# Kernel optimization log

Measured on AMD Instinct MI355X. Metric: run time of the kernel, lower is better.

The kernel has to match this reference:

```python
import jax, jax.numpy as jnp
import numpy as np

T = 200000


def _sine_layer(tvec, A, w, phi, phic, wc):
    # tvec: (t,), A/w/phi: (n,1), phic/wc: (1,)
    phi_static = jax.nn.relu(phic)  # (1,)
    w_static = jax.nn.relu(wc)
    ph = jax.nn.relu(phi) + phi_static  # (n,1)
    ww = jax.nn.relu(w) + w_static
    sine = A * jnp.sin(ww * tvec[None, :] + ph)  # (n,t)
    return sine, phi_static, w_static


def _selector_layer(tvec, wave_input, w, phi, phic, wc, phi_prev, w_prev):
    # wave_input: (n,t), w/phi: (m,n), phic/wc/phi_prev/w_prev: (1,)
    # NOTE: phi_prev/w_prev passed but phi_prev flag is False in the network,
    # so they are NOT added (matches torch: `if self.phi_prev and ...`).
    phi_static = jax.nn.relu(phic)
    w_static = jax.nn.relu(wc)
    ph = (jax.nn.relu(phi) + phi_static)[:, :, None]  # (m,n,1)
    ww = (jax.nn.relu(w) + w_static)[:, :, None]
    sine = 0.5 * jnp.sin(ww * tvec[None, None, :] + ph) + 0.5  # (m,n,t)
    out = jnp.einsum('mnt,nt->mt', sine, wave_input)  # (m,t)
    return out, phi_static, w_static


def setup_inputs() -> dict:
    key = jax.random.key(0)
    ks = jax.random.split(key, 18)
    r = lambda k, s: jax.random.normal(k, s, dtype=jnp.float32)
    return {
        'initial_wave_input': r(ks[0], (20, T)),
        'A0': r(ks[1], (20, 1)), 'w0': r(ks[2], (20, 1)), 'phi0': r(ks[3], (20, 1)),
        'wc0': r(ks[4], (1,)), 'phic0': r(ks[5], (1,)),
        'w1': r(ks[6], (25, 20)), 'phi1': r(ks[7], (25, 20)),
        'wc1': r(ks[8], (1,)), 'phic1': r(ks[9], (1,)),
        'w2': r(ks[10], (30, 25)), 'phi2': r(ks[11], (30, 25)),
        'wc2': r(ks[12], (1,)), 'phic2': r(ks[13], (1,)),
        'w3': r(ks[14], (1, 30)), 'phi3': r(ks[15], (1, 30)),
        'wc3': r(ks[16], (1,)), 'phic3': r(ks[17], (1,)),
    }


def reference(initial_wave_input, A0, w0, phi0, wc0, phic0,
              w1, phi1, wc1, phic1, w2, phi2, wc2, phic2,
              w3, phi3, wc3, phic3):
    tvec = jnp.linspace(1.0, 1000.0, T, dtype=jnp.float32)
    # initial_wave_input is an argument of the torch module but is never used.
    s, phi, w = _sine_layer(tvec, A0, w0, phi0, phic0, wc0)
    s, phi, w = _selector_layer(tvec, s, w1, phi1, phic1, wc1, phi, w)
    s, phi, w = _selector_layer(tvec, s, w2, phi2, phic2, wc2, phi, w)
    s, phi, w = _selector_layer(tvec, s, w3, phi3, phic3, wc3, phi, w)
    return s  # (1, t)
```

## Files before the change

kernel.cpp:

```cpp
#include <hip/hip_runtime.h>
#include <hip/hip_bf16.h>

#define T_TOTAL 200000
#define T_PAD   200192
#define STEPF   (999.0f / 199999.0f)

typedef float v4f __attribute__((ext_vector_type(4)));

__device__ float g_P[5200];
__device__ float g_s1[25 * T_PAD];

__device__ __forceinline__ float sinp(float rev) {
    float g = __builtin_amdgcn_fractf(rev);
    float h = g - 0.5f;
    float u = h * h;
    float p = fmaf(45.621248f, u, -82.391040f);
    p = fmaf(p, u, 64.671616f);
    p = fmaf(p, u, -19.730960f);
    p = fmaf(p, u, 0.9999618f);
    return p;
}

__global__ void prep_kernel(
    const float* __restrict__ A0,
    const float* __restrict__ w0, const float* __restrict__ phi0,
    const float* __restrict__ wc0, const float* __restrict__ phic0,
    const float* __restrict__ w1, const float* __restrict__ phi1,
    const float* __restrict__ wc1, const float* __restrict__ phic1,
    const float* __restrict__ w2, const float* __restrict__ phi2,
    const float* __restrict__ wc2, const float* __restrict__ phic2,
    const float* __restrict__ w3, const float* __restrict__ phi3,
    const float* __restrict__ wc3, const float* __restrict__ phic3)
{
    const int tid = blockIdx.x * blockDim.x + threadIdx.x;
    const int stride = blockDim.x * gridDim.x;

    const double I2PI = 0.15915494309189535;
    const double D64  = 64.0 * 999.0 / 199999.0;

    const double ws0 = fmax((double)wc0[0], 0.0), ps0 = fmax((double)phic0[0], 0.0);
    const double ws1 = fmax((double)wc1[0], 0.0), ps1 = fmax((double)phic1[0], 0.0);
    const double ws2 = fmax((double)wc2[0], 0.0), ps2 = fmax((double)phic2[0], 0.0);
    const double ws3 = fmax((double)wc3[0], 0.0), ps3 = fmax((double)phic3[0], 0.0);

    for (int n = tid; n < 20; n += stride) {
        double wr = fmax((double)w0[n], 0.0) + ws0;
        g_P[4 * n]     = (float)(wr * I2PI);
        g_P[4 * n + 1] = (float)((fmax((double)phi0[n], 0.0) + ps0) * I2PI + 0.25);
        g_P[4 * n + 2] = (float)(2.0 * cos(wr * D64));
        g_P[4 * n + 3] = A0[n];
    }
    for (int k = tid; k < 25 * 20; k += stride) {
        double wr = fmax((double)w1[k], 0.0) + ws1;
        g_P[80 + 4 * k]     = (float)(wr * I2PI);
        g_P[80 + 4 * k + 1] = (float)((fmax((double)phi1[k], 0.0) + ps1) * I2PI + 0.25);
        g_P[80 + 4 * k + 2] = (float)(2.0 * cos(wr * D64));
        g_P[80 + 4 * k + 3] = 0.0f;
    }
    for (int k = tid; k < 30 * 25; k += stride) {
        double wr = fmax((double)w2[k], 0.0) + ws2;
        g_P[2080 + 4 * k]     = (float)(wr * I2PI);
        g_P[2080 + 4 * k + 1] = (float)((fmax((double)phi2[k], 0.0) + ps2) * I2PI + 0.25);
        g_P[2080 + 4 * k + 2] = (float)(2.0 * cos(wr * D64));
        g_P[2080 + 4 * k + 3] = 0.0f;
    }
    for (int m = tid; m < 30; m += stride) {
        double wr = fmax((double)w3[m], 0.0) + ws3;
        g_P[5080 + 4 * m]     = (float)(wr * I2PI);
        g_P[5080 + 4 * m + 1] = (float)((fmax((double)phi3[m], 0.0) + ps3) * I2PI + 0.25);
        g_P[5080 + 4 * m + 2] = (float)(2.0 * cos(wr * D64));
        g_P[5080 + 4 * m + 3] = 0.0f;
    }
}

__launch_bounds__(256)
__global__ void k_l01()
{
    __shared__ float P[2080];
    __shared__ float s0s[20 * 256];

    for (int i = threadIdx.x; i < 2080; i += 256) P[i] = g_P[i];

    const int l = threadIdx.x & 63;
    const int w = __builtin_amdgcn_readfirstlane(threadIdx.x >> 6);
    const int tb = blockIdx.x * 256;
    const float tv0 = fmaf((float)(tb + l), STEPF, 1.0f);
    const float tv1 = fmaf((float)(tb + l + 64), STEPF, 1.0f);

#pragma unroll
    for (int i = 0; i < 5; ++i) {
        const int n = 5 * w + i;
        const v4f q = *(const v4f*)&g_P[4 * n];
        float x0 = q[3] * sinp(fmaf(q[0], tv0, q[1]));
        float x1 = q[3] * sinp(fmaf(q[0], tv1, q[1]));
        float x2 = fmaf(q[2], x1, -x0);
        float x3 = fmaf(q[2], x2, -x1);
        s0s[n * 256 +       l] = x0;
        s0s[n * 256 +  64 + l] = x1;
        s0s[n * 256 + 128 + l] = x2;
        s0s[n * 256 + 192 + l] = x3;
    }
    __syncthreads();

    float sum0[4] = {0.f, 0.f, 0.f, 0.f};
#pragma unroll
    for (int n = 0; n < 20; ++n) {
        sum0[0] += s0s[n * 256 +       l];
        sum0[1] += s0s[n * 256 +  64 + l];
        sum0[2] += s0s[n * 256 + 128 + l];
        sum0[3] += s0s[n * 256 + 192 + l];
    }

    const int mS = w ? (1 + 6 * w) : 0;
    const int mC = w ? 6 : 7;
    for (int i = 0; i < mC; ++i) {
        const int m = mS + i;
        float a0 = 0.f, a1 = 0.f, a2 = 0.f, a3 = 0.f;
        const float* __restrict__ pb = &P[80 + 80 * m];
#pragma unroll
        for (int n = 0; n < 20; ++n) {
            const v4f q = *(const v4f*)&pb[4 * n];
            const float s00 = s0s[n * 256 +       l];
            const float s01 = s0s[n * 256 +  64 + l];
            const float s02 = s0s[n * 256 + 128 + l];
            const float s03 = s0s[n * 256 + 192 + l];
            float x0 = sinp(fmaf(q[0], tv0, q[1]));
            float x1 = sinp(fmaf(q[0], tv1, q[1]));
            float x2 = fmaf(q[2], x1, -x0);
            float x3 = fmaf(q[2], x2, -x1);
            a0 = fmaf(x0, s00, a0);
            a1 = fmaf(x1, s01, a1);
            a2 = fmaf(x2, s02, a2);
            a3 = fmaf(x3, s03, a3);
        }
        float* __restrict__ o = &g_s1[m * T_PAD + tb];
        o[l]       = fmaf(0.5f, a0, 0.5f * sum0[0]);
        o[64 + l]  = fmaf(0.5f, a1, 0.5f * sum0[1]);
        o[128 + l] = fmaf(0.5f, a2, 0.5f * sum0[2]);
        o[192 + l] = fmaf(0.5f, a3, 0.5f * sum0[3]);
    }
}

__launch_bounds__(256)
__global__ void k_l23(float* __restrict__ out)
{
    __shared__ float P[3120];
    __shared__ float s1s[25 * 256];
    __shared__ float shp[16 * 64];

    const int tb = blockIdx.x * 256;
    for (int i = threadIdx.x; i < 3120; i += 256) P[i] = g_P[2080 + i];
    for (int i = threadIdx.x; i < 25 * 256; i += 256) {
        const int n = i >> 8;
        s1s[i] = g_s1[n * T_PAD + tb + (i & 255)];
    }
    __syncthreads();

    const int l = threadIdx.x & 63;
    const int w = __builtin_amdgcn_readfirstlane(threadIdx.x >> 6);
    const float tv0 = fmaf((float)(tb + l), STEPF, 1.0f);
    const float tv1 = fmaf((float)(tb + l + 64), STEPF, 1.0f);

    float sum1[4] = {0.f, 0.f, 0.f, 0.f};
#pragma unroll
    for (int n = 0; n < 25; ++n) {
        sum1[0] += s1s[n * 256 +       l];
        sum1[1] += s1s[n * 256 +  64 + l];
        sum1[2] += s1s[n * 256 + 128 + l];
        sum1[3] += s1s[n * 256 + 192 + l];
    }

    const int mS = (w < 2) ? 8 * w : (16 + 7 * (w - 2));
    const int mC = (w < 2) ? 8 : 7;
    float p0 = 0.f, p1 = 0.f, p2 = 0.f, p3 = 0.f;
    for (int i = 0; i < mC; ++i) {
        const int m = mS + i;
        float a0 = 0.f, a1 = 0.f, a2 = 0.f, a3 = 0.f;
        const float* __restrict__ pb = &P[100 * m];
#pragma unroll
        for (int n = 0; n < 25; ++n) {
            const v4f q = *(const v4f*)&pb[4 * n];
            const float s10 = s1s[n * 256 +       l];
            const float s11 = s1s[n * 256 +  64 + l];
            const float s12 = s1s[n * 256 + 128 + l];
            const float s13 = s1s[n * 256 + 192 + l];
            float x0 = sinp(fmaf(q[0], tv0, q[1]));
            float x1 = sinp(fmaf(q[0], tv1, q[1]));
            float x2 = fmaf(q[2], x1, -x0);
            float x3 = fmaf(q[2], x2, -x1);
            a0 = fmaf(x0, s10, a0);
            a1 = fmaf(x1, s11, a1);
            a2 = fmaf(x2, s12, a2);
            a3 = fmaf(x3, s13, a3);
        }
        const v4f q3 = *(const v4f*)&P[3000 + 4 * m];
        float y0 = sinp(fmaf(q3[0], tv0, q3[1]));
        float y1 = sinp(fmaf(q3[0], tv1, q3[1]));
        float y2 = fmaf(q3[2], y1, -y0);
        float y3 = fmaf(q3[2], y2, -y1);
        p0 = fmaf(fmaf(0.5f, y0, 0.5f), fmaf(0.5f, a0, 0.5f * sum1[0]), p0);
        p1 = fmaf(fmaf(0.5f, y1, 0.5f), fmaf(0.5f, a1, 0.5f * sum1[1]), p1);
        p2 = fmaf(fmaf(0.5f, y2, 0.5f), fmaf(0.5f, a2, 0.5f * sum1[2]), p2);
        p3 = fmaf(fmaf(0.5f, y3, 0.5f), fmaf(0.5f, a3, 0.5f * sum1[3]), p3);
    }
    shp[(w * 4 + 0) * 64 + l] = p0;
    shp[(w * 4 + 1) * 64 + l] = p1;
    shp[(w * 4 + 2) * 64 + l] = p2;
    shp[(w * 4 + 3) * 64 + l] = p3;
    __syncthreads();

    const float r = (shp[(0 * 4 + w) * 64 + l] + shp[(1 * 4 + w) * 64 + l])
                  + (shp[(2 * 4 + w) * 64 + l] + shp[(3 * 4 + w) * 64 + l]);
    const int tt = tb + 64 * w + l;
    if (tt < T_TOTAL) out[tt] = r;
}

extern "C" void kernel_launch(void* const* d_in, const int* in_sizes, int n_in,
                              void* d_out, int out_size, void* d_ws, size_t ws_size,
                              hipStream_t stream) {
    (void)in_sizes; (void)n_in; (void)d_ws; (void)ws_size; (void)out_size;
    const float* A0    = (const float*)d_in[1];
    const float* w0    = (const float*)d_in[2];
    const float* phi0  = (const float*)d_in[3];
    const float* wc0   = (const float*)d_in[4];
    const float* phic0 = (const float*)d_in[5];
    const float* w1    = (const float*)d_in[6];
    const float* phi1  = (const float*)d_in[7];
    const float* wc1   = (const float*)d_in[8];
    const float* phic1 = (const float*)d_in[9];
    const float* w2    = (const float*)d_in[10];
    const float* phi2  = (const float*)d_in[11];
    const float* wc2   = (const float*)d_in[12];
    const float* phic2 = (const float*)d_in[13];
    const float* w3    = (const float*)d_in[14];
    const float* phi3  = (const float*)d_in[15];
    const float* wc3   = (const float*)d_in[16];
    const float* phic3 = (const float*)d_in[17];

    float* out = (float*)d_out;

    hipLaunchKernelGGL(prep_kernel, dim3(6), dim3(256), 0, stream,
                       A0, w0, phi0, wc0, phic0,
                       w1, phi1, wc1, phic1,
                       w2, phi2, wc2, phic2,
                       w3, phi3, wc3, phic3);

    const int grid = (T_TOTAL + 255) / 256;
    hipLaunchKernelGGL(k_l01, dim3(grid), dim3(256), 0, stream);
    hipLaunchKernelGGL(k_l23, dim3(grid), dim3(256), 0, stream, out);
}
```

Measured before the change: 62.53 us.

## Use 512-thread blocks with 4-way output register blocking in both layer kernels

Both kernels now run 8 waves per 256-timestep block. Each wave computes up to four output channels together, so every selector input value loaded is reused across four accumulators. The layer-2/3 kernel stops staging the intermediate into shared memory and reads it straight from global memory, and the final reduction now combines 8 wave partials. In exchange, layer 1 does redundant work on overlapping or clamped channels (32 slots for 25 channels, plus duplicated layer-0 sines), and the launch bounds request higher occupancy, which may push register pressure.

```diff
diff --git a/kernel.cpp b/kernel.cpp
--- a/kernel.cpp
+++ b/kernel.cpp
@@ -73,13 +73,13 @@
     }
 }
 
-__launch_bounds__(256)
+__launch_bounds__(512, 8)
 __global__ void k_l01()
 {
-    __shared__ float P[2080];
+    __shared__ float pp[2000];
     __shared__ float s0s[20 * 256];
 
-    for (int i = threadIdx.x; i < 2080; i += 256) P[i] = g_P[i];
+    for (int i = threadIdx.x; i < 2000; i += 512) pp[i] = g_P[80 + i];
 
     const int l = threadIdx.x & 63;
     const int w = __builtin_amdgcn_readfirstlane(threadIdx.x >> 6);
@@ -87,132 +87,143 @@
     const float tv0 = fmaf((float)(tb + l), STEPF, 1.0f);
     const float tv1 = fmaf((float)(tb + l + 64), STEPF, 1.0f);
 
-#pragma unroll
-    for (int i = 0; i < 5; ++i) {
-        const int n = 5 * w + i;
-        const v4f q = *(const v4f*)&g_P[4 * n];
-        float x0 = q[3] * sinp(fmaf(q[0], tv0, q[1]));
-        float x1 = q[3] * sinp(fmaf(q[0], tv1, q[1]));
-        float x2 = fmaf(q[2], x1, -x0);
-        float x3 = fmaf(q[2], x2, -x1);
-        s0s[n * 256 +       l] = x0;
-        s0s[n * 256 +  64 + l] = x1;
-        s0s[n * 256 + 128 + l] = x2;
-        s0s[n * 256 + 192 + l] = x3;
+    {
+        const int nn0 = w, nn1 = 8 + w, nn2 = (16 + w < 20) ? 16 + w : 19;
+        const int nn[3] = {nn0, nn1, nn2};
+#pragma unroll
+        for (int i = 0; i < 3; ++i) {
+            const int n = nn[i];
+            const v4f q = *(const v4f*)&g_P[4 * n];
+            float x0 = q[3] * sinp(fmaf(q[0], tv0, q[1]));
+            float x1 = q[3] * sinp(fmaf(q[0], tv1, q[1]));
+            float x2 = fmaf(q[2], x1, -x0);
+            float x3 = fmaf(q[2], x2, -x1);
+            s0s[n * 256 +       l] = x0;
+            s0s[n * 256 +  64 + l] = x1;
+            s0s[n * 256 + 128 + l] = x2;
+            s0s[n * 256 + 192 + l] = x3;
+        }
     }
     __syncthreads();
 
+    int m_[4];
+#pragma unroll
+    for (int i = 0; i < 4; ++i) {
+        int m = (25 * w) / 8 + i;
+        m_[i] = (m > 24) ? 24 : m;
+    }
+
+    float acc[4][4] = {};
     float sum0[4] = {0.f, 0.f, 0.f, 0.f};
-#pragma unroll
+#pragma clang loop unroll_count(2)
     for (int n = 0; n < 20; ++n) {
-        sum0[0] += s0s[n * 256 +       l];
-        sum0[1] += s0s[n * 256 +  64 + l];
-        sum0[2] += s0s[n * 256 + 128 + l];
-        sum0[3] += s0s[n * 256 + 192 + l];
-    }
-
-    const int mS = w ? (1 + 6 * w) : 0;
-    const int mC = w ? 6 : 7;
-    for (int i = 0; i < mC; ++i) {
-        const int m = mS + i;
-        float a0 = 0.f, a1 = 0.f, a2 = 0.f, a3 = 0.f;
-        const float* __restrict__ pb = &P[80 + 80 * m];
-#pragma unroll
-        for (int n = 0; n < 20; ++n) {
-            const v4f q = *(const v4f*)&pb[4 * n];
-            const float s00 = s0s[n * 256 +       l];
-            const float s01 = s0s[n * 256 +  64 + l];
-            const float s02 = s0s[n * 256 + 128 + l];
-            const float s03 = s0s[n * 256 + 192 + l];
+        const float s00 = s0s[n * 256 +       l];
+        const float s01 = s0s[n * 256 +  64 + l];
+        const float s02 = s0s[n * 256 + 128 + l];
+        const float s03 = s0s[n * 256 + 192 + l];
+        sum0[0] += s00; sum0[1] += s01; sum0[2] += s02; sum0[3] += s03;
+#pragma unroll
+        for (int i = 0; i < 4; ++i) {
+            const v4f q = *(const v4f*)&pp[4 * (m_[i] * 20 + n)];
             float x0 = sinp(fmaf(q[0], tv0, q[1]));
             float x1 = sinp(fmaf(q[0], tv1, q[1]));
             float x2 = fmaf(q[2], x1, -x0);
             float x3 = fmaf(q[2], x2, -x1);
-            a0 = fmaf(x0, s00, a0);
-            a1 = fmaf(x1, s01, a1);
-            a2 = fmaf(x2, s02, a2);
-            a3 = fmaf(x3, s03, a3);
+            acc[i][0] = fmaf(x0, s00, acc[i][0]);
+            acc[i][1] = fmaf(x1, s01, acc[i][1]);
+            acc[i][2] = fmaf(x2, s02, acc[i][2]);
+            acc[i][3] = fmaf(x3, s03, acc[i][3]);
         }
-        float* __restrict__ o = &g_s1[m * T_PAD + tb];
-        o[l]       = fmaf(0.5f, a0, 0.5f * sum0[0]);
-        o[64 + l]  = fmaf(0.5f, a1, 0.5f * sum0[1]);
-        o[128 + l] = fmaf(0.5f, a2, 0.5f * sum0[2]);
-        o[192 + l] = fmaf(0.5f, a3, 0.5f * sum0[3]);
-    }
-}
-
-__launch_bounds__(256)
+    }
+#pragma unroll
+    for (int i = 0; i < 4; ++i) {
+        float* __restrict__ o = &g_s1[m_[i] * T_PAD + tb];
+        o[l]       = fmaf(0.5f, acc[i][0], 0.5f * sum0[0]);
+        o[64 + l]  = fmaf(0.5f, acc[i][1], 0.5f * sum0[1]);
+        o[128 + l] = fmaf(0.5f, acc[i][2], 0.5f * sum0[2]);
+        o[192 + l] = fmaf(0.5f, acc[i][3], 0.5f * sum0[3]);
+    }
+}
+
+__launch_bounds__(512, 8)
 __global__ void k_l23(float* __restrict__ out)
 {
-    __shared__ float P[3120];
-    __shared__ float s1s[25 * 256];
-    __shared__ float shp[16 * 64];
-
-    const int tb = blockIdx.x * 256;
-    for (int i = threadIdx.x; i < 3120; i += 256) P[i] = g_P[2080 + i];
-    for (int i = threadIdx.x; i < 25 * 256; i += 256) {
-        const int n = i >> 8;
-        s1s[i] = g_s1[n * T_PAD + tb + (i & 255)];
-    }
+    __shared__ float pp[3120];
+    __shared__ float shp[8 * 4 * 64];
+
+    for (int i = threadIdx.x; i < 3120; i += 512) pp[i] = g_P[2080 + i];
     __syncthreads();
 
     const int l = threadIdx.x & 63;
     const int w = __builtin_amdgcn_readfirstlane(threadIdx.x >> 6);
+    const int tb = blockIdx.x * 256;
     const float tv0 = fmaf((float)(tb + l), STEPF, 1.0f);
     const float tv1 = fmaf((float)(tb + l + 64), STEPF, 1.0f);
 
+    const int mS = (30 * w) / 8;
+    const int mE = (30 * (w + 1)) / 8;
+    int m_[4]; float fl[4];
+#pragma unroll
+    for (int i = 0; i < 4; ++i) {
+        int m = mS + i;
+        fl[i] = (m < mE) ? 1.0f : 0.0f;
+        m_[i] = (m > 29) ? 29 : m;
+    }
+
+    float acc[4][4] = {};
     float sum1[4] = {0.f, 0.f, 0.f, 0.f};
-#pragma unroll
+#pragma clang loop unroll_count(2)
     for (int n = 0; n < 25; ++n) {
-        sum1[0] += s1s[n * 256 +       l];
-        sum1[1] += s1s[n * 256 +  64 + l];
-        sum1[2] += s1s[n * 256 + 128 + l];
-        sum1[3] += s1s[n * 256 + 192 + l];
-    }
-
-    const int mS = (w < 2) ? 8 * w : (16 + 7 * (w - 2));
-    const int mC = (w < 2) ? 8 : 7;
-    float p0 = 0.f, p1 = 0.f, p2 = 0.f, p3 = 0.f;
-    for (int i = 0; i < mC; ++i) {
-        const int m = mS + i;
-        float a0 = 0.f, a1 = 0.f, a2 = 0.f, a3 = 0.f;
-        const float* __restrict__ pb = &P[100 * m];
-#pragma unroll
-        for (int n = 0; n < 25; ++n) {
-            const v4f q = *(const v4f*)&pb[4 * n];
-            const float s10 = s1s[n * 256 +       l];
-            const float s11 = s1s[n * 256 +  64 + l];
-            const float s12 = s1s[n * 256 + 128 + l];
-            const float s13 = s1s[n * 256 + 192 + l];
+        const float* __restrict__ sp = &g_s1[n * T_PAD + tb];
+        const float s10 = sp[l];
+        const float s11 = sp[64 + l];
+        const float s12 = sp[128 + l];
+        const float s13 = sp[192 + l];
+        sum1[0] += s10; sum1[1] += s11; sum1[2] += s12; sum1[3] += s13;
+#pragma unroll
+        for (int i = 0; i < 4; ++i) {
+            const v4f q = *(const v4f*)&pp[4 * (m_[i] * 25 + n)];
             float x0 = sinp(fmaf(q[0], tv0, q[1]));
             float x1 = sinp(fmaf(q[0], tv1, q[1]));
             float x2 = fmaf(q[2], x1, -x0);
             float x3 = fmaf(q[2], x2, -x1);
-            a0 = fmaf(x0, s10, a0);
-            a1 = fmaf(x1, s11, a1);
-            a2 = fmaf(x2, s12, a2);
-            a3 = fmaf(x3, s13, a3);
+            acc[i][0] = fmaf(x0, s10, acc[i][0]);
+            acc[i][1] = fmaf(x1, s11, acc[i][1]);
+            acc[i][2] = fmaf(x2, s12, acc[i][2]);
+            acc[i][3] = fmaf(x3, s13, acc[i][3]);
         }
-        const v4f q3 = *(const v4f*)&P[3000 + 4 * m];
+    }
+
+    float pw[4] = {0.f, 0.f, 0.f, 0.f};
+#pragma unroll
+    for (int i = 0; i < 4; ++i) {
+        const v4f q3 = *(const v4f*)&pp[3000 + 4 * m_[i]];
         float y0 = sinp(fmaf(q3[0], tv0, q3[1]));
         float y1 = sinp(fmaf(q3[0], tv1, q3[1]));
         float y2 = fmaf(q3[2], y1, -y0);
         float y3 = fmaf(q3[2], y2, -y1);
-        p0 = fmaf(fmaf(0.5f, y0, 0.5f), fmaf(0.5f, a0, 0.5f * sum1[0]), p0);
-        p1 = fmaf(fmaf(0.5f, y1, 0.5f), fmaf(0.5f, a1, 0.5f * sum1[1]), p1);
-        p2 = fmaf(fmaf(0.5f, y2, 0.5f), fmaf(0.5f, a2, 0.5f * sum1[2]), p2);
-        p3 = fmaf(fmaf(0.5f, y3, 0.5f), fmaf(0.5f, a3, 0.5f * sum1[3]), p3);
-    }
-    shp[(w * 4 + 0) * 64 + l] = p0;
-    shp[(w * 4 + 1) * 64 + l] = p1;
-    shp[(w * 4 + 2) * 64 + l] = p2;
-    shp[(w * 4 + 3) * 64 + l] = p3;
+        const float s20 = fmaf(0.5f, acc[i][0], 0.5f * sum1[0]);
+        const float s21 = fmaf(0.5f, acc[i][1], 0.5f * sum1[1]);
+        const float s22 = fmaf(0.5f, acc[i][2], 0.5f * sum1[2]);
+        const float s23 = fmaf(0.5f, acc[i][3], 0.5f * sum1[3]);
+        pw[0] = fmaf(fl[i] * fmaf(0.5f, y0, 0.5f), s20, pw[0]);
+        pw[1] = fmaf(fl[i] * fmaf(0.5f, y1, 0.5f), s21, pw[1]);
+        pw[2] = fmaf(fl[i] * fmaf(0.5f, y2, 0.5f), s22, pw[2]);
+        pw[3] = fmaf(fl[i] * fmaf(0.5f, y3, 0.5f), s23, pw[3]);
+    }
+#pragma unroll
+    for (int j = 0; j < 4; ++j)
+        shp[(w * 4 + j) * 64 + l] = pw[j];
     __syncthreads();
 
-    const float r = (shp[(0 * 4 + w) * 64 + l] + shp[(1 * 4 + w) * 64 + l])
-                  + (shp[(2 * 4 + w) * 64 + l] + shp[(3 * 4 + w) * 64 + l]);
-    const int tt = tb + 64 * w + l;
-    if (tt < T_TOTAL) out[tt] = r;
+    if (w < 4) {
+        float r = 0.0f;
+#pragma unroll
+        for (int w2 = 0; w2 < 8; ++w2)
+            r += shp[(w2 * 4 + w) * 64 + l];
+        const int tt = tb + 64 * w + l;
+        if (tt < T_TOTAL) out[tt] = r;
+    }
 }
 
 extern "C" void kernel_launch(void* const* d_in, const int* in_sizes, int n_in,
@@ -246,6 +257,6 @@
                        w3, phi3, wc3, phic3);
 
     const int grid = (T_TOTAL + 255) / 256;
-    hipLaunchKernelGGL(k_l01, dim3(grid), dim3(256), 0, stream);
-    hipLaunchKernelGGL(k_l23, dim3(grid), dim3(256), 0, stream, out);
-}
+    hipLaunchKernelGGL(k_l01, dim3(grid), dim3(512), 0, stream);
+    hipLaunchKernelGGL(k_l23, dim3(grid), dim3(512), 0, stream, out);
+}
```

Result: no change. 62.58 us (+0.1%).

## Assign each lane four consecutive time points and vectorize shared/global accesses

Applied to the files above, without the earlier changes.

Each lane now handles four adjacent time samples instead of four samples spaced 64 apart, so the Chebyshev recurrence coefficient uses a single-step cosine and the per-lane activations can be read and written as 128-bit vectors in LDS and global memory. The layer-0 parameters are no longer copied into shared memory, and the final reduction buffer reuses the parameter LDS area after an extra barrier, which lowers shared-memory footprint. Adjacent-step recurrence accumulates less error per step but changes the float rounding, and wide LDS accesses with a 16-byte lane stride may change the bank-conflict pattern.

```diff
diff --git a/kernel.cpp b/kernel.cpp
--- a/kernel.cpp
+++ b/kernel.cpp
@@ -36,7 +36,7 @@
     const int stride = blockDim.x * gridDim.x;
 
     const double I2PI = 0.15915494309189535;
-    const double D64  = 64.0 * 999.0 / 199999.0;
+    const double D1   = 999.0 / 199999.0;
 
     const double ws0 = fmax((double)wc0[0], 0.0), ps0 = fmax((double)phic0[0], 0.0);
     const double ws1 = fmax((double)wc1[0], 0.0), ps1 = fmax((double)phic1[0], 0.0);
@@ -47,28 +47,28 @@
         double wr = fmax((double)w0[n], 0.0) + ws0;
         g_P[4 * n]     = (float)(wr * I2PI);
         g_P[4 * n + 1] = (float)((fmax((double)phi0[n], 0.0) + ps0) * I2PI + 0.25);
-        g_P[4 * n + 2] = (float)(2.0 * cos(wr * D64));
+        g_P[4 * n + 2] = (float)(2.0 * cos(wr * D1));
         g_P[4 * n + 3] = A0[n];
     }
     for (int k = tid; k < 25 * 20; k += stride) {
         double wr = fmax((double)w1[k], 0.0) + ws1;
         g_P[80 + 4 * k]     = (float)(wr * I2PI);
         g_P[80 + 4 * k + 1] = (float)((fmax((double)phi1[k], 0.0) + ps1) * I2PI + 0.25);
-        g_P[80 + 4 * k + 2] = (float)(2.0 * cos(wr * D64));
+        g_P[80 + 4 * k + 2] = (float)(2.0 * cos(wr * D1));
         g_P[80 + 4 * k + 3] = 0.0f;
     }
     for (int k = tid; k < 30 * 25; k += stride) {
         double wr = fmax((double)w2[k], 0.0) + ws2;
         g_P[2080 + 4 * k]     = (float)(wr * I2PI);
         g_P[2080 + 4 * k + 1] = (float)((fmax((double)phi2[k], 0.0) + ps2) * I2PI + 0.25);
-        g_P[2080 + 4 * k + 2] = (float)(2.0 * cos(wr * D64));
+        g_P[2080 + 4 * k + 2] = (float)(2.0 * cos(wr * D1));
         g_P[2080 + 4 * k + 3] = 0.0f;
     }
     for (int m = tid; m < 30; m += stride) {
         double wr = fmax((double)w3[m], 0.0) + ws3;
         g_P[5080 + 4 * m]     = (float)(wr * I2PI);
         g_P[5080 + 4 * m + 1] = (float)((fmax((double)phi3[m], 0.0) + ps3) * I2PI + 0.25);
-        g_P[5080 + 4 * m + 2] = (float)(2.0 * cos(wr * D64));
+        g_P[5080 + 4 * m + 2] = (float)(2.0 * cos(wr * D1));
         g_P[5080 + 4 * m + 3] = 0.0f;
     }
 }
@@ -76,16 +76,18 @@
 __launch_bounds__(256)
 __global__ void k_l01()
 {
-    __shared__ float P[2080];
+    __shared__ float pp[2000];
     __shared__ float s0s[20 * 256];
 
-    for (int i = threadIdx.x; i < 2080; i += 256) P[i] = g_P[i];
-
-    const int l = threadIdx.x & 63;
-    const int w = __builtin_amdgcn_readfirstlane(threadIdx.x >> 6);
+    const int tid = threadIdx.x;
+    for (int i = tid; i < 2000; i += 256) pp[i] = g_P[80 + i];
+
+    const int l = tid & 63;
+    const int w = __builtin_amdgcn_readfirstlane(tid >> 6);
     const int tb = blockIdx.x * 256;
-    const float tv0 = fmaf((float)(tb + l), STEPF, 1.0f);
-    const float tv1 = fmaf((float)(tb + l + 64), STEPF, 1.0f);
+    const int tl = 4 * l;
+    const float tv0 = fmaf((float)(tb + tl), STEPF, 1.0f);
+    const float tv1 = tv0 + STEPF;
 
 #pragma unroll
     for (int i = 0; i < 5; ++i) {
@@ -95,123 +97,109 @@
         float x1 = q[3] * sinp(fmaf(q[0], tv1, q[1]));
         float x2 = fmaf(q[2], x1, -x0);
         float x3 = fmaf(q[2], x2, -x1);
-        s0s[n * 256 +       l] = x0;
-        s0s[n * 256 +  64 + l] = x1;
-        s0s[n * 256 + 128 + l] = x2;
-        s0s[n * 256 + 192 + l] = x3;
+        *(v4f*)&s0s[n * 256 + tl] = (v4f){x0, x1, x2, x3};
     }
     __syncthreads();
 
     float sum0[4] = {0.f, 0.f, 0.f, 0.f};
 #pragma unroll
     for (int n = 0; n < 20; ++n) {
-        sum0[0] += s0s[n * 256 +       l];
-        sum0[1] += s0s[n * 256 +  64 + l];
-        sum0[2] += s0s[n * 256 + 128 + l];
-        sum0[3] += s0s[n * 256 + 192 + l];
+        const v4f s = *(const v4f*)&s0s[n * 256 + tl];
+        sum0[0] += s[0]; sum0[1] += s[1]; sum0[2] += s[2]; sum0[3] += s[3];
     }
 
     const int mS = w ? (1 + 6 * w) : 0;
     const int mC = w ? 6 : 7;
     for (int i = 0; i < mC; ++i) {
         const int m = mS + i;
+        const float* __restrict__ pb = &pp[80 * m];
         float a0 = 0.f, a1 = 0.f, a2 = 0.f, a3 = 0.f;
-        const float* __restrict__ pb = &P[80 + 80 * m];
 #pragma unroll
         for (int n = 0; n < 20; ++n) {
             const v4f q = *(const v4f*)&pb[4 * n];
-            const float s00 = s0s[n * 256 +       l];
-            const float s01 = s0s[n * 256 +  64 + l];
-            const float s02 = s0s[n * 256 + 128 + l];
-            const float s03 = s0s[n * 256 + 192 + l];
+            const v4f s = *(const v4f*)&s0s[n * 256 + tl];
             float x0 = sinp(fmaf(q[0], tv0, q[1]));
             float x1 = sinp(fmaf(q[0], tv1, q[1]));
             float x2 = fmaf(q[2], x1, -x0);
             float x3 = fmaf(q[2], x2, -x1);
-            a0 = fmaf(x0, s00, a0);
-            a1 = fmaf(x1, s01, a1);
-            a2 = fmaf(x2, s02, a2);
-            a3 = fmaf(x3, s03, a3);
+            a0 = fmaf(x0, s[0], a0);
+            a1 = fmaf(x1, s[1], a1);
+            a2 = fmaf(x2, s[2], a2);
+            a3 = fmaf(x3, s[3], a3);
         }
-        float* __restrict__ o = &g_s1[m * T_PAD + tb];
-        o[l]       = fmaf(0.5f, a0, 0.5f * sum0[0]);
-        o[64 + l]  = fmaf(0.5f, a1, 0.5f * sum0[1]);
-        o[128 + l] = fmaf(0.5f, a2, 0.5f * sum0[2]);
-        o[192 + l] = fmaf(0.5f, a3, 0.5f * sum0[3]);
+        const v4f o = {fmaf(0.5f, a0, 0.5f * sum0[0]),
+                       fmaf(0.5f, a1, 0.5f * sum0[1]),
+                       fmaf(0.5f, a2, 0.5f * sum0[2]),
+                       fmaf(0.5f, a3, 0.5f * sum0[3])};
+        *(v4f*)&g_s1[m * T_PAD + tb + tl] = o;
     }
 }
 
 __launch_bounds__(256)
 __global__ void k_l23(float* __restrict__ out)
 {
-    __shared__ float P[3120];
+    __shared__ float pp[3120];
     __shared__ float s1s[25 * 256];
-    __shared__ float shp[16 * 64];
-
+
+    const int tid = threadIdx.x;
     const int tb = blockIdx.x * 256;
-    for (int i = threadIdx.x; i < 3120; i += 256) P[i] = g_P[2080 + i];
-    for (int i = threadIdx.x; i < 25 * 256; i += 256) {
-        const int n = i >> 8;
-        s1s[i] = g_s1[n * T_PAD + tb + (i & 255)];
-    }
-    __syncthreads();
-
-    const int l = threadIdx.x & 63;
-    const int w = __builtin_amdgcn_readfirstlane(threadIdx.x >> 6);
-    const float tv0 = fmaf((float)(tb + l), STEPF, 1.0f);
-    const float tv1 = fmaf((float)(tb + l + 64), STEPF, 1.0f);
+    for (int i = tid; i < 3120; i += 256) pp[i] = g_P[2080 + i];
+    for (int i = tid; i < 25 * 256; i += 256)
+        s1s[i] = g_s1[(i >> 8) * T_PAD + tb + (i & 255)];
+    __syncthreads();
+
+    const int l = tid & 63;
+    const int w = __builtin_amdgcn_readfirstlane(tid >> 6);
+    const int tl = 4 * l;
+    const float tv0 = fmaf((float)(tb + tl), STEPF, 1.0f);
+    const float tv1 = tv0 + STEPF;
 
     float sum1[4] = {0.f, 0.f, 0.f, 0.f};
 #pragma unroll
     for (int n = 0; n < 25; ++n) {
-        sum1[0] += s1s[n * 256 +       l];
-        sum1[1] += s1s[n * 256 +  64 + l];
-        sum1[2] += s1s[n * 256 + 128 + l];
-        sum1[3] += s1s[n * 256 + 192 + l];
+        const v4f s = *(const v4f*)&s1s[n * 256 + tl];
+        sum1[0] += s[0]; sum1[1] += s[1]; sum1[2] += s[2]; sum1[3] += s[3];
     }
 
     const int mS = (w < 2) ? 8 * w : (16 + 7 * (w - 2));
     const int mC = (w < 2) ? 8 : 7;
-    float p0 = 0.f, p1 = 0.f, p2 = 0.f, p3 = 0.f;
+    float pw0 = 0.f, pw1 = 0.f, pw2 = 0.f, pw3 = 0.f;
     for (int i = 0; i < mC; ++i) {
         const int m = mS + i;
+        const float* __restrict__ pb = &pp[100 * m];
         float a0 = 0.f, a1 = 0.f, a2 = 0.f, a3 = 0.f;
-        const float* __restrict__ pb = &P[100 * m];
 #pragma unroll
         for (int n = 0; n < 25; ++n) {
             const v4f q = *(const v4f*)&pb[4 * n];
-            const float s10 = s1s[n * 256 +       l];
-            const float s11 = s1s[n * 256 +  64 + l];
-            const float s12 = s1s[n * 256 + 128 + l];
-            const float s13 = s1s[n * 256 + 192 + l];
+            const v4f s = *(const v4f*)&s1s[n * 256 + tl];
             float x0 = sinp(fmaf(q[0], tv0, q[1]));
             float x1 = sinp(fmaf(q[0], tv1, q[1]));
             float x2 = fmaf(q[2], x1, -x0);
             float x3 = fmaf(q[2], x2, -x1);
-            a0 = fmaf(x0, s10, a0);
-            a1 = fmaf(x1, s11, a1);
-            a2 = fmaf(x2, s12, a2);
-            a3 = fmaf(x3, s13, a3);
+            a0 = fmaf(x0, s[0], a0);
+            a1 = fmaf(x1, s[1], a1);
+            a2 = fmaf(x2, s[2], a2);
+            a3 = fmaf(x3, s[3], a3);
         }
-        const v4f q3 = *(const v4f*)&P[3000 + 4 * m];
+        const v4f q3 = *(const v4f*)&pp[3000 + 4 * m];
         float y0 = sinp(fmaf(q3[0], tv0, q3[1]));
         float y1 = sinp(fmaf(q3[0], tv1, q3[1]));
         float y2 = fmaf(q3[2], y1, -y0);
         float y3 = fmaf(q3[2], y2, -y1);
-        p0 = fmaf(fmaf(0.5f, y0, 0.5f), fmaf(0.5f, a0, 0.5f * sum1[0]), p0);
-        p1 = fmaf(fmaf(0.5f, y1, 0.5f), fmaf(0.5f, a1, 0.5f * sum1[1]), p1);
-        p2 = fmaf(fmaf(0.5f, y2, 0.5f), fmaf(0.5f, a2, 0.5f * sum1[2]), p2);
-        p3 = fmaf(fmaf(0.5f, y3, 0.5f), fmaf(0.5f, a3, 0.5f * sum1[3]), p3);
-    }
-    shp[(w * 4 + 0) * 64 + l] = p0;
-    shp[(w * 4 + 1) * 64 + l] = p1;
-    shp[(w * 4 + 2) * 64 + l] = p2;
-    shp[(w * 4 + 3) * 64 + l] = p3;
-    __syncthreads();
-
-    const float r = (shp[(0 * 4 + w) * 64 + l] + shp[(1 * 4 + w) * 64 + l])
-                  + (shp[(2 * 4 + w) * 64 + l] + shp[(3 * 4 + w) * 64 + l]);
-    const int tt = tb + 64 * w + l;
+        pw0 = fmaf(fmaf(0.5f, y0, 0.5f), fmaf(0.5f, a0, 0.5f * sum1[0]), pw0);
+        pw1 = fmaf(fmaf(0.5f, y1, 0.5f), fmaf(0.5f, a1, 0.5f * sum1[1]), pw1);
+        pw2 = fmaf(fmaf(0.5f, y2, 0.5f), fmaf(0.5f, a2, 0.5f * sum1[2]), pw2);
+        pw3 = fmaf(fmaf(0.5f, y3, 0.5f), fmaf(0.5f, a3, 0.5f * sum1[3]), pw3);
+    }
+    __syncthreads();
+    float* const shp = pp;
+    *(v4f*)&shp[w * 256 + tl] = (v4f){pw0, pw1, pw2, pw3};
+    __syncthreads();
+
+    const int tlr = 64 * w + l;
+    const float r = (shp[0 * 256 + tlr] + shp[1 * 256 + tlr])
+                  + (shp[2 * 256 + tlr] + shp[3 * 256 + tlr]);
+    const int tt = tb + tlr;
     if (tt < T_TOTAL) out[tt] = r;
 }
 
```

Result: slower. 64.68 us (+3.4%).
